# Optimization experiments

Measured on AMD Instinct MI355X. Metric: run time of the kernel, lower is better.

## Reference

```python
import jax, jax.numpy as jnp
import numpy as np

B, LQ, E = 4, 8400, 256
HEADS, LEVELS, POINTS = 8, 4, 4
HEAD_DIM = E // HEADS
SHAPES = [(80, 80), (40, 40), (20, 20), (10, 10)]  # (H, W) per level; sum HW = 8400
LV = sum(h * w for h, w in SHAPES)


def setup_inputs() -> dict:
    key = jax.random.key(0)
    ks = jax.random.split(key, 12)
    query = jax.random.normal(ks[0], (B, LQ, E), jnp.float32)
    # per-level normalized reference points in (0.1, 0.9)
    reference_points = 0.1 + 0.8 * jax.random.uniform(ks[1], (B, LQ, LEVELS, 2), jnp.float32)
    value = jax.random.normal(ks[2], (B, LV, E), jnp.float32)
    spatial_shapes = jnp.array(SHAPES, dtype=jnp.int32)
    s = 0.05
    Wv = jax.random.normal(ks[3], (E, E), jnp.float32) * s
    bv = jnp.zeros((E,), jnp.float32)
    Woff = jax.random.normal(ks[4], (E, HEADS * LEVELS * POINTS * 2), jnp.float32) * 0.01
    boff = jax.random.normal(ks[5], (HEADS * LEVELS * POINTS * 2,), jnp.float32) * 0.02
    Wattn = jax.random.normal(ks[6], (E, HEADS * LEVELS * POINTS), jnp.float32) * s
    battn = jnp.zeros((HEADS * LEVELS * POINTS,), jnp.float32)
    Wo = jax.random.normal(ks[7], (E, E), jnp.float32) * s
    bo = jnp.zeros((E,), jnp.float32)
    return dict(query=query, reference_points=reference_points, value=value,
                spatial_shapes=spatial_shapes, Wv=Wv, bv=bv, Woff=Woff, boff=boff,
                Wattn=Wattn, battn=battn, Wo=Wo, bo=bo)


def _bilinear_sample(vflat, x, y, Hl, Wl):
    # vflat: [BH, D, Hl*Wl]; x, y: [BH, N] pixel coords (align_corners=False convention)
    x0f = jnp.floor(x); y0f = jnp.floor(y)
    wx = (x - x0f)[:, None, :]; wy = (y - y0f)[:, None, :]
    x0 = x0f.astype(jnp.int32); y0 = y0f.astype(jnp.int32)

    def gather(ix, iy):
        valid = ((ix >= 0) & (ix < Wl) & (iy >= 0) & (iy < Hl)).astype(vflat.dtype)
        idx = jnp.clip(iy, 0, Hl - 1) * Wl + jnp.clip(ix, 0, Wl - 1)
        g = jnp.take_along_axis(vflat, idx[:, None, :], axis=2)  # [BH, D, N]
        return g * valid[:, None, :]

    v00 = gather(x0, y0); v01 = gather(x0 + 1, y0)
    v10 = gather(x0, y0 + 1); v11 = gather(x0 + 1, y0 + 1)
    return (v00 * (1 - wx) * (1 - wy) + v01 * wx * (1 - wy)
            + v10 * (1 - wx) * wy + v11 * wx * wy)


def _msda_forward(query, reference_points, value, spatial_shapes,
                  Wv, bv, Woff, boff, Wattn, battn, Wo, bo):
    b, lq, _ = query.shape
    v = (value @ Wv + bv).reshape(b, -1, HEADS, HEAD_DIM)
    off = (query @ Woff + boff).reshape(b, lq, HEADS, LEVELS, POINTS, 2)
    aw = (query @ Wattn + battn).reshape(b, lq, HEADS, LEVELS * POINTS)
    aw = jax.nn.softmax(aw, axis=-1).reshape(b, lq, HEADS, LEVELS, POINTS)
    # normalizer (W, H) per level
    norm = jnp.stack([spatial_shapes[:, 1], spatial_shapes[:, 0]], axis=-1).astype(query.dtype)
    # sampling locations in [0,1]: [B, Lq, H, L, P, 2]
    loc = reference_points[:, :, None, :, None, :] + off / norm[None, None, None, :, None, :]

    sampled_levels = []
    start = 0
    for lvl, (Hl, Wl) in enumerate(SHAPES):
        vl = v[:, start:start + Hl * Wl]                      # [B, Hl*Wl, H, D]
        start += Hl * Wl
        vflat = vl.transpose(0, 2, 3, 1).reshape(b * HEADS, HEAD_DIM, Hl * Wl)
        grid = loc[:, :, :, lvl]                              # [B, Lq, H, P, 2]
        grid = grid.transpose(0, 2, 1, 3, 4).reshape(b * HEADS, lq * POINTS, 2)
        g = grid * 2.0 - 1.0                                  # grid_sample convention
        x = (g[..., 0] + 1.0) * (Wl * 0.5) - 0.5
        y = (g[..., 1] + 1.0) * (Hl * 0.5) - 0.5
        s = _bilinear_sample(vflat, x, y, Hl, Wl)             # [BH, D, Lq*P]
        sampled_levels.append(s.reshape(b, HEADS, HEAD_DIM, lq, POINTS))
    sampled = jnp.stack(sampled_levels, axis=-1)              # [B, H, D, Lq, P, L]
    out = jnp.einsum('bhdqpl,bqhlp->bqhd', sampled, aw).reshape(b, lq, E)
    return out @ Wo + bo


def reference(query, reference_points, value, spatial_shapes,
              Wv, bv, Woff, boff, Wattn, battn, Wo, bo):
    return _msda_forward(query, reference_points, value, spatial_shapes,
                         Wv, bv, Woff, boff, Wattn, battn, Wo, bo)
```

## Files before the change

kernel.cpp:

```cpp
#include <hip/hip_runtime.h>
#include <math.h>

#define BB 4
#define LQ 8400
#define NH 8
#define LVTOT 8500
#define HD 32
#define PLANE_USH 544000

typedef __attribute__((ext_vector_type(8))) short short8;
typedef __attribute__((ext_vector_type(4))) float f32x4;
typedef __attribute__((ext_vector_type(2))) _Float16 half2_t;
typedef __attribute__((ext_vector_type(2))) __fp16 fp16x2_t;
typedef unsigned short ushort_t;

__device__ __forceinline__ ushort_t f2bf(float f) {
    union { float f; unsigned u; } v; v.f = f;
    unsigned r = v.u + 0x7fffu + ((v.u >> 16) & 1u);
    return (ushort_t)(r >> 16);
}
__device__ __forceinline__ float bflo(unsigned u) {
    union { unsigned u; float f; } x; x.u = u << 16; return x.f;
}
__device__ __forceinline__ float bfhi(unsigned u) {
    union { unsigned u; float f; } x; x.u = u & 0xffff0000u; return x.f;
}
__device__ __forceinline__ half2_t ash2(unsigned u) {
    union { unsigned u; half2_t h; } x; x.u = u; return x.h;
}
__device__ __forceinline__ unsigned pk2u(fp16x2_t h) {
    union { fp16x2_t h; unsigned u; } x; x.h = h; return x.u;
}

__device__ __forceinline__ void dma16(const ushort_t* g, ushort_t* l) {
    __builtin_amdgcn_global_load_lds(
        (const __attribute__((address_space(1))) void*)g,
        (__attribute__((address_space(3))) void*)l, 16, 0, 0);
}

__device__ __forceinline__ void lvl_decomp(int pix, int& lb, int& y, int& x,
                                           int& rowp) {
    if (pix < 6400)      { y = pix / 80;            x = pix - y * 80;  rowp = 40; lb = 0; }
    else if (pix < 8000) { int r = pix - 6400; y = r / 40; x = r - y * 40; rowp = 20; lb = 3200; }
    else if (pix < 8400) { int r = pix - 8000; y = r / 20; x = r - y * 20; rowp = 10; lb = 4000; }
    else                 { int r = pix - 8400; y = r / 10; x = r - y * 10; rowp = 5;  lb = 4200; }
}

__global__ __launch_bounds__(256) void prep_all(
    const float* __restrict__ value, const float* __restrict__ query,
    const float* __restrict__ Wv, const float* __restrict__ Woff,
    const float* __restrict__ Wattn, const float* __restrict__ Wo,
    ushort_t* __restrict__ value_b, ushort_t* __restrict__ query_b,
    ushort_t* __restrict__ BT)
{
    const int bid = blockIdx.x;
    if (bid < 16900) {
        const float* src = (bid < 8500) ? value : query;
        ushort_t* dst = (bid < 8500) ? value_b : query_b;
        int i = (bid < 8500 ? bid : bid - 8500) * 256 + threadIdx.x;
        float4 f = ((const float4*)src)[i];
        ushort4 o;
        o.x = f2bf(f.x); o.y = f2bf(f.y); o.z = f2bf(f.z); o.w = f2bf(f.w);
        ((ushort4*)dst)[i] = o;
    } else {
        int idx = (bid - 16900) * 256 + threadIdx.x;
        int r = idx >> 8, k = idx & 255;
        float v;
        if (r < 256) v = Wv[k * 256 + r];
        else if (r < 640) {
            int n = r - 256;
            v = (n < 256) ? Woff[k * 256 + n] : Wattn[k * 128 + (n - 256)];
        } else v = Wo[k * 256 + (r - 640)];
        BT[idx] = f2bf(v);
    }
}

__device__ __forceinline__ void gemm_core64(
    const ushort_t* __restrict__ A, const ushort_t* __restrict__ B, int M,
    int m0, int n0, ushort_t* Asl, ushort_t* Bsl, f32x4 acc[2][4])
{
    const int tid  = threadIdx.x;
    const int wave = tid >> 6, lane = tid & 63;
    const int quad = lane >> 4, mr = lane & 15;
    const int wm   = (wave >> 1) * 32, wn = (wave & 1) * 64;
    const int oct  = lane >> 3;
    const int bseg = lane & 7;

    for (int k0 = 0; k0 < 256; k0 += 64) {
        __syncthreads();
        #pragma unroll
        for (int i = 0; i < 2; i++) {
            int m  = i * 32 + wave * 8 + oct;
            int gs = bseg ^ (m & 7);
            int am = min(m0 + m, M - 1);
            dma16(A + (size_t)am * 256 + k0 + gs * 8,
                  Asl + (i * 32 + wave * 8) * 64 + lane * 8);
        }
        #pragma unroll
        for (int i = 0; i < 4; i++) {
            int n  = i * 32 + wave * 8 + oct;
            int gs = bseg ^ (n & 7);
            dma16(B + (size_t)(n0 + n) * 256 + k0 + gs * 8,
                  Bsl + (i * 32 + wave * 8) * 64 + lane * 8);
        }
        __syncthreads();
        #pragma unroll
        for (int ks = 0; ks < 2; ks++) {
            short8 af[2], bf[4];
            const int ksl = ks * 4 + quad;
            #pragma unroll
            for (int i = 0; i < 2; i++) {
                int m = wm + i * 16 + mr;
                af[i] = *(const short8*)&Asl[m * 64 + (ksl ^ (m & 7)) * 8];
            }
            #pragma unroll
            for (int j = 0; j < 4; j++) {
                int n = wn + j * 16 + mr;
                bf[j] = *(const short8*)&Bsl[n * 64 + (ksl ^ (n & 7)) * 8];
            }
            #pragma unroll
            for (int i = 0; i < 2; i++)
                #pragma unroll
                for (int j = 0; j < 4; j++)
                    acc[i][j] = __builtin_amdgcn_mfma_f32_16x16x32_bf16(
                        af[i], bf[j], acc[i][j], 0, 0, 0);
        }
    }
}

__global__ __launch_bounds__(256, 4) void gemm_fused(
    const ushort_t* __restrict__ Av, const ushort_t* __restrict__ Aq,
    const ushort_t* __restrict__ BT,
    const float* __restrict__ bv, const float* __restrict__ boff,
    const float* __restrict__ battn,
    ushort_t* __restrict__ vperm, ushort_t* __restrict__ off_b,
    ushort_t* __restrict__ awl_b)
{
    __shared__ ushort_t smem[12288];
    ushort_t* Asl = smem;
    ushort_t* Bsl = smem + 4096;

    const int bid = blockIdx.x;
    int mode, m0, n0, M;
    const ushort_t *A, *B;
    if (bid < 1064) { mode = 0; m0 = (bid >> 1) * 64; n0 = (bid & 1) * 128;
                      A = Av; B = BT; M = 34000; }
    else { int b2 = bid - 1064;
           mode = 1; m0 = (b2 / 3) * 64; n0 = (b2 % 3) * 128;
           A = Aq; B = BT + 65536; M = 33600; }

    f32x4 acc[2][4];
    #pragma unroll
    for (int i = 0; i < 2; i++)
        #pragma unroll
        for (int j = 0; j < 4; j++) acc[i][j] = (f32x4){0.f, 0.f, 0.f, 0.f};

    gemm_core64(A, B, M, m0, n0, Asl, Bsl, acc);

    const int tid  = threadIdx.x;
    const int wave = tid >> 6, lane = tid & 63;
    const int quad = lane >> 4, mr = lane & 15;
    const int wm   = (wave >> 1) * 32, wn = (wave & 1) * 64;

    __syncthreads();
    #pragma unroll
    for (int i = 0; i < 2; i++) {
        #pragma unroll
        for (int j = 0; j < 4; j++) {
            const int lc = wn + j * 16 + mr;
            const int c  = n0 + lc;
            const float bias = (mode == 0) ? bv[c]
                              : (c < 256 ? boff[c] : battn[c - 256]);
            #pragma unroll
            for (int reg = 0; reg < 4; reg++) {
                const int rl = wm + i * 16 + quad * 4 + reg;
                float val = acc[i][j][reg] + bias;
                ushort_t u;
                if (mode == 0) { union { _Float16 h; ushort_t u; } cv;
                                 cv.h = (_Float16)val; u = cv.u; }
                else u = f2bf(val);
                smem[rl * 128 + (lc ^ ((rl & 3) << 3))] = u;
            }
        }
    }
    __syncthreads();

    if (mode == 1) {
        #pragma unroll
        for (int k = 0; k < 4; k++) {
            int sid = k * 256 + tid;
            int rl = sid >> 4, cc = (sid & 15) * 8;
            int row = m0 + rl;
            if (row >= M) continue;
            uint4 v = *(const uint4*)&smem[rl * 128 + (cc ^ ((rl & 3) << 3))];
            if (n0 < 256) *(uint4*)&off_b[(size_t)row * 256 + n0 + cc] = v;
            else          *(uint4*)&awl_b[(size_t)row * 128 + cc] = v;
        }
    } else {
        const int hb = n0 >> 5;
        #pragma unroll
        for (int k = 0; k < 8; k++) {
            int sid = k * 256 + tid;
            int unit = sid >> 5;
            if (unit >= 63) continue;
            int sub = sid & 31;
            int hh = sub >> 3, q = sub & 7;
            int copy = (unit >= 32) ? 1 : 0;
            int t = copy ? ((unit - 32) * 2 + 1) : (unit * 2);
            int row = m0 + t;
            if (row + 1 >= 34000) continue;
            int b = row / LVTOT, pix = row - b * LVTOT;
            int lb, y, x, rowp;
            lvl_decomp(pix, lb, y, x, rowp);
            if (copy && x >= 2 * rowp - 1) continue;
            int p = x >> 1;
            int pidx = copy * 4250 + lb + y * rowp + p;
            int h = hb + hh;
            uint2 a  = *(const uint2*)&smem[t * 128 +
                          ((hh * 32 + q * 4) ^ ((t & 3) << 3))];
            uint2 b2 = *(const uint2*)&smem[(t + 1) * 128 +
                          ((hh * 32 + q * 4) ^ (((t + 1) & 3) << 3))];
            uint4 o;
            o.x = (a.x & 0xffffu) | (b2.x << 16);
            o.y = (a.x >> 16)     | (b2.x & 0xffff0000u);
            o.z = (a.y & 0xffffu) | (b2.y << 16);
            o.w = (a.y >> 16)     | (b2.y & 0xffff0000u);
            *(uint4*)((char*)(vperm + (size_t)(b * NH + h) * PLANE_USH)
                      + (size_t)pidx * 128 + q * 16) = o;
        }
        {
            int pixsel = tid >> 7;
            int rem = tid & 127;
            int hh = rem >> 5, d = rem & 31;
            int t = pixsel ? 63 : 0;
            int row = m0 + t;
            if (row < 34000) {
                int b = row / LVTOT, pix = row - b * LVTOT;
                int lb, y, x, rowp;
                lvl_decomp(pix, lb, y, x, rowp);
                bool doit; int p, slot;
                if (!pixsel) { doit = (x >= 2);            p = (x - 2) >> 1; slot = 1; }
                else         { doit = (x < 2 * rowp - 1);  p = (x - 1) >> 1; slot = 0; }
                if (doit) {
                    int pidx = 4250 + lb + y * rowp + p;
                    int h = hb + hh;
                    vperm[(size_t)(b * NH + h) * PLANE_USH
                          + (size_t)pidx * 64 + d * 2 + slot] =
                        smem[t * 128 + ((hh * 32 + d) ^ ((t & 3) << 3))];
                }
            }
        }
    }
}

__global__ __launch_bounds__(256, 4) void gemm_out(
    const ushort_t* __restrict__ A, const ushort_t* __restrict__ BT,
    const float* __restrict__ bo, float* __restrict__ out)
{
    __shared__ ushort_t smem[12288];
    ushort_t* Asl = smem;
    ushort_t* Bsl = smem + 4096;

    const int m0 = (blockIdx.x >> 1) * 64;
    const int n0 = (blockIdx.x & 1) * 128;
    const int M = 33600;

    f32x4 acc[2][4];
    #pragma unroll
    for (int i = 0; i < 2; i++)
        #pragma unroll
        for (int j = 0; j < 4; j++) acc[i][j] = (f32x4){0.f, 0.f, 0.f, 0.f};

    gemm_core64(A, BT, M, m0, n0, Asl, Bsl, acc);

    const int tid  = threadIdx.x;
    const int wave = tid >> 6, lane = tid & 63;
    const int quad = lane >> 4, mr = lane & 15;
    const int half = wave >> 1;
    const int wn   = (wave & 1) * 64;
    float* fsm = (float*)smem;

    #pragma unroll
    for (int i = 0; i < 2; i++) {
        __syncthreads();
        #pragma unroll
        for (int j = 0; j < 4; j++) {
            const int lc = wn + j * 16 + mr;
            const float bias = bo[n0 + lc];
            #pragma unroll
            for (int reg = 0; reg < 4; reg++) {
                const int rloc = half * 16 + quad * 4 + reg;
                const int cs = lc ^ (quad << 4);
                fsm[rloc * 128 + cs] = acc[i][j][reg] + bias;
            }
        }
        __syncthreads();
        #pragma unroll
        for (int k = 0; k < 4; k++) {
            int sid = k * 256 + tid;
            int rloc = sid >> 5, cw = (sid & 31) * 4;
            int row = m0 + (rloc >> 4) * 32 + i * 16 + (rloc & 15);
            if (row >= M) continue;
            int q2 = (rloc >> 2) & 3;
            float4 v = *(const float4*)&fsm[rloc * 128 + (cw ^ (q2 << 4))];
            *(float4*)&out[(size_t)row * 256 + n0 + cw] = v;
        }
    }
}

__global__ __launch_bounds__(256) void msda_sample(
    const ushort_t* __restrict__ vperm, const ushort_t* __restrict__ off,
    const ushort_t* __restrict__ awl, const float* __restrict__ refp,
    ushort_t* __restrict__ sampled)
{
    __shared__ int4 s_wi[16 * 33];

    const int tid = threadIdx.x;
    const int bid = blockIdx.x;
    const int h   = bid & 7;
    const int r   = bid >> 3;
    const int b   = r / 263;
    const int c   = r - b * 263;
    const int q0b = c * 32;
    const size_t bq0 = (size_t)b * LQ + q0b;

    const int Hs[4]    = {80, 40, 20, 10};
    const int pbase[4] = {0, 3200, 4000, 4200};

    #pragma unroll
    for (int it = 0; it < 2; it++) {
        const int s  = it * 256 + tid;
        const int ql = s >> 4, lp = s & 15;
        const int l  = lp >> 2;
        const int qv = (q0b + ql < LQ) ? ql : 0;
        const size_t bq = bq0 + qv;
        const int Wl = Hs[l];

        unsigned od = *(const unsigned*)(off + bq * 256 + h * 32 + lp * 2);
        float ox = bflo(od), oy = bfhi(od);
        float lgt = bflo((unsigned)awl[bq * 128 + h * 16 + lp]);
        float e = __expf(lgt);
        float sum = e;
        sum += __shfl_xor(sum, 1, 16);
        sum += __shfl_xor(sum, 2, 16);
        sum += __shfl_xor(sum, 4, 16);
        sum += __shfl_xor(sum, 8, 16);
        float aw = e * __builtin_amdgcn_rcpf(sum);

        float2 rp = *(const float2*)(refp + bq * 8 + l * 2);
        float x = rp.x * (float)Wl + ox - 0.5f;
        float y = rp.y * (float)Wl + oy - 0.5f;
        float x0f = floorf(x), y0f = floorf(y);
        float wx = x - x0f, wy = y - y0f;
        int x0 = (int)x0f, y0 = (int)y0f;
        float hx0 = ((x0 >= 0) & (x0 < Wl)) ? (1.f - wx) : 0.f;
        float hx1 = ((x0 + 1 >= 0) & (x0 + 1 < Wl)) ? wx : 0.f;
        float vy0w = ((y0 >= 0) & (y0 < Wl)) ? (1.f - wy) * aw : 0.f;
        float vy1w = ((y0 + 1 >= 0) & (y0 + 1 < Wl)) ? wy * aw : 0.f;
        int px = min(max(x0, 0), Wl - 2);
        float pl, pr;
        if (x0 < px)      { pl = hx1; pr = 0.f; }
        else if (x0 > px) { pl = 0.f; pr = hx0; }
        else              { pl = hx0; pr = hx1; }
        int cy0 = min(max(y0, 0), Wl - 1);
        int cy1 = min(max(y0 + 1, 0), Wl - 1);
        const int copy = px & 1;
        const int p    = copy ? ((px - 1) >> 1) : (px >> 1);
        const int rowp = Wl >> 1;
        const int cb   = copy * 4250 + pbase[l] + p;
        const int otop = (cb + cy0 * rowp) << 7;
        const int obot = (cb + cy1 * rowp) << 7;
        unsigned wt = pk2u(__builtin_amdgcn_cvt_pkrtz(pl * vy0w, pr * vy0w));
        unsigned wb = pk2u(__builtin_amdgcn_cvt_pkrtz(pl * vy1w, pr * vy1w));
        s_wi[lp * 33 + ql] = make_int4((int)wt, (int)wb, otop, obot);
    }
    __syncthreads();

    const int ql  = tid >> 3;
    const int l8  = tid & 7;
    const int dby = l8 * 16;

    if (q0b + ql < LQ) {
        const char* plane = (const char*)(vperm + (size_t)(b * NH + h) * PLANE_USH);
        float a0 = 0.f, a1 = 0.f, a2 = 0.f, a3 = 0.f;
        #pragma unroll
        for (int pt = 0; pt < 16; pt++) {
            int4 wi = s_wi[pt * 33 + ql];
            uint4 vt = *(const uint4*)(plane + (unsigned)(wi.z + dby));
            uint4 vb = *(const uint4*)(plane + (unsigned)(wi.w + dby));
            half2_t wt = ash2((unsigned)wi.x);
            half2_t wb = ash2((unsigned)wi.y);
            a0 = __builtin_amdgcn_fdot2(wt, ash2(vt.x), a0, false);
            a0 = __builtin_amdgcn_fdot2(wb, ash2(vb.x), a0, false);
            a1 = __builtin_amdgcn_fdot2(wt, ash2(vt.y), a1, false);
            a1 = __builtin_amdgcn_fdot2(wb, ash2(vb.y), a1, false);
            a2 = __builtin_amdgcn_fdot2(wt, ash2(vt.z), a2, false);
            a2 = __builtin_amdgcn_fdot2(wb, ash2(vb.z), a2, false);
            a3 = __builtin_amdgcn_fdot2(wt, ash2(vt.w), a3, false);
            a3 = __builtin_amdgcn_fdot2(wb, ash2(vb.w), a3, false);
        }
        const size_t bq = bq0 + ql;
        ushort4 o;
        o.x = f2bf(a0); o.y = f2bf(a1);
        o.z = f2bf(a2); o.w = f2bf(a3);
        *(ushort4*)(sampled + bq * 256 + h * 32 + l8 * 4) = o;
    }
}

extern "C" void kernel_launch(void* const* d_in, const int* in_sizes, int n_in,
                              void* d_out, int out_size, void* d_ws, size_t ws_size,
                              hipStream_t stream) {
    const float* query = (const float*)d_in[0];
    const float* refp  = (const float*)d_in[1];
    const float* value = (const float*)d_in[2];
    const float* Wv    = (const float*)d_in[4];
    const float* bv    = (const float*)d_in[5];
    const float* Woff  = (const float*)d_in[6];
    const float* boff  = (const float*)d_in[7];
    const float* Wattn = (const float*)d_in[8];
    const float* battn = (const float*)d_in[9];
    const float* Wo    = (const float*)d_in[10];
    const float* bo    = (const float*)d_in[11];
    float* out = (float*)d_out;

    ushort_t* ws = (ushort_t*)d_ws;
    ushort_t* off_b   = ws;
    ushort_t* awl_b   = off_b + 8601600;
    ushort_t* value_b = awl_b + 4300800;
    ushort_t* query_b = value_b + 8704000;
    ushort_t* vperm_b = query_b + 8601600;
    ushort_t* BT      = vperm_b + 17408000;
    ushort_t* sampled_b = query_b;

    prep_all<<<dim3(17796), 256, 0, stream>>>(
        value, query, Wv, Woff, Wattn, Wo, value_b, query_b, BT);

    gemm_fused<<<dim3(1064 + 1575), 256, 0, stream>>>(
        value_b, query_b, BT, bv, boff, battn, vperm_b, off_b, awl_b);

    msda_sample<<<dim3(8 * 4 * 263), 256, 0, stream>>>(
        vperm_b, off_b, awl_b, refp, sampled_b);

    gemm_out<<<dim3(1050), 256, 0, stream>>>(
        sampled_b, BT + 163840, bo, out);
}
```

Baseline: 209.5 us.

## Fuse fp32-to-bf16 input conversion into the projection GEMM A-tile load

The separate pass that converted value and query to bf16 is removed. The GEMM now DMAs fp32 A tiles straight into LDS with an XOR swizzle and converts them to bf16 in registers just before the MFMA. This drops one full read and write of both activation tensors plus a prep pass over them, leaving only the small weight-transpose prep kernel. In exchange the GEMM moves twice as many A bytes from global memory, uses more LDS (which may lower occupancy), and does the conversion arithmetic inside the inner loop.

```diff
diff --git a/kernel.cpp b/kernel.cpp
--- a/kernel.cpp
+++ b/kernel.cpp
@@ -37,6 +37,11 @@
         (const __attribute__((address_space(1))) void*)g,
         (__attribute__((address_space(3))) void*)l, 16, 0, 0);
 }
+__device__ __forceinline__ void dma16g(const void* g, void* l) {
+    __builtin_amdgcn_global_load_lds(
+        (const __attribute__((address_space(1))) void*)g,
+        (__attribute__((address_space(3))) void*)l, 16, 0, 0);
+}
 
 __device__ __forceinline__ void lvl_decomp(int pix, int& lb, int& y, int& x,
                                            int& rowp) {
@@ -46,32 +51,83 @@
     else                 { int r = pix - 8400; y = r / 10; x = r - y * 10; rowp = 5;  lb = 4200; }
 }
 
-__global__ __launch_bounds__(256) void prep_all(
-    const float* __restrict__ value, const float* __restrict__ query,
+__global__ __launch_bounds__(256) void prep_bt(
     const float* __restrict__ Wv, const float* __restrict__ Woff,
     const float* __restrict__ Wattn, const float* __restrict__ Wo,
-    ushort_t* __restrict__ value_b, ushort_t* __restrict__ query_b,
     ushort_t* __restrict__ BT)
 {
-    const int bid = blockIdx.x;
-    if (bid < 16900) {
-        const float* src = (bid < 8500) ? value : query;
-        ushort_t* dst = (bid < 8500) ? value_b : query_b;
-        int i = (bid < 8500 ? bid : bid - 8500) * 256 + threadIdx.x;
-        float4 f = ((const float4*)src)[i];
-        ushort4 o;
-        o.x = f2bf(f.x); o.y = f2bf(f.y); o.z = f2bf(f.z); o.w = f2bf(f.w);
-        ((ushort4*)dst)[i] = o;
-    } else {
-        int idx = (bid - 16900) * 256 + threadIdx.x;
-        int r = idx >> 8, k = idx & 255;
-        float v;
-        if (r < 256) v = Wv[k * 256 + r];
-        else if (r < 640) {
-            int n = r - 256;
-            v = (n < 256) ? Woff[k * 256 + n] : Wattn[k * 128 + (n - 256)];
-        } else v = Wo[k * 256 + (r - 640)];
-        BT[idx] = f2bf(v);
+    int idx = blockIdx.x * 256 + threadIdx.x;
+    int r = idx >> 8, k = idx & 255;
+    float v;
+    if (r < 256) v = Wv[k * 256 + r];
+    else if (r < 640) {
+        int n = r - 256;
+        v = (n < 256) ? Woff[k * 256 + n] : Wattn[k * 128 + (n - 256)];
+    } else v = Wo[k * 256 + (r - 640)];
+    BT[idx] = f2bf(v);
+}
+
+__device__ __forceinline__ void gemm_core64_f32a(
+    const float* __restrict__ A, const ushort_t* __restrict__ B, int M,
+    int m0, int n0, float* Af, ushort_t* Bsl, f32x4 acc[2][4])
+{
+    const int tid  = threadIdx.x;
+    const int wave = tid >> 6, lane = tid & 63;
+    const int quad = lane >> 4, mr = lane & 15;
+    const int wm   = (wave >> 1) * 32, wn = (wave & 1) * 64;
+    const int oct  = lane >> 3;
+    const int bseg = lane & 7;
+    const int r4   = lane >> 4;
+    const int s16  = lane & 15;
+
+    for (int k0 = 0; k0 < 256; k0 += 64) {
+        __syncthreads();
+        #pragma unroll
+        for (int i = 0; i < 4; i++) {
+            int m  = i * 16 + wave * 4 + r4;
+            int gs = s16 ^ (m & 15);
+            int am = min(m0 + m, M - 1);
+            dma16g((const char*)A + (size_t)am * 1024 + (size_t)(k0 + gs * 4) * 4,
+                   (char*)Af + (i * 16 + wave * 4) * 256 + lane * 16);
+        }
+        #pragma unroll
+        for (int i = 0; i < 4; i++) {
+            int n  = i * 32 + wave * 8 + oct;
+            int gs = bseg ^ (n & 7);
+            dma16(B + (size_t)(n0 + n) * 256 + k0 + gs * 8,
+                  Bsl + (i * 32 + wave * 8) * 64 + lane * 8);
+        }
+        __syncthreads();
+        #pragma unroll
+        for (int ks = 0; ks < 2; ks++) {
+            short8 af[2], bf[4];
+            const int ksl = ks * 4 + quad;
+            #pragma unroll
+            for (int i = 0; i < 2; i++) {
+                int m  = wm + i * 16 + mr;
+                int p0 = (ksl * 2) ^ (m & 15);
+                int p1 = (ksl * 2 + 1) ^ (m & 15);
+                float4 lo = *(const float4*)&Af[m * 64 + p0 * 4];
+                float4 hi = *(const float4*)&Af[m * 64 + p1 * 4];
+                short8 a;
+                a[0] = (short)f2bf(lo.x); a[1] = (short)f2bf(lo.y);
+                a[2] = (short)f2bf(lo.z); a[3] = (short)f2bf(lo.w);
+                a[4] = (short)f2bf(hi.x); a[5] = (short)f2bf(hi.y);
+                a[6] = (short)f2bf(hi.z); a[7] = (short)f2bf(hi.w);
+                af[i] = a;
+            }
+            #pragma unroll
+            for (int j = 0; j < 4; j++) {
+                int n = wn + j * 16 + mr;
+                bf[j] = *(const short8*)&Bsl[n * 64 + (ksl ^ (n & 7)) * 8];
+            }
+            #pragma unroll
+            for (int i = 0; i < 2; i++)
+                #pragma unroll
+                for (int j = 0; j < 4; j++)
+                    acc[i][j] = __builtin_amdgcn_mfma_f32_16x16x32_bf16(
+                        af[i], bf[j], acc[i][j], 0, 0, 0);
+        }
     }
 }
 
@@ -129,20 +185,21 @@
 }
 
 __global__ __launch_bounds__(256, 4) void gemm_fused(
-    const ushort_t* __restrict__ Av, const ushort_t* __restrict__ Aq,
+    const float* __restrict__ Av, const float* __restrict__ Aq,
     const ushort_t* __restrict__ BT,
     const float* __restrict__ bv, const float* __restrict__ boff,
     const float* __restrict__ battn,
     ushort_t* __restrict__ vperm, ushort_t* __restrict__ off_b,
     ushort_t* __restrict__ awl_b)
 {
-    __shared__ ushort_t smem[12288];
-    ushort_t* Asl = smem;
-    ushort_t* Bsl = smem + 4096;
+    __shared__ ushort_t smem[16384];
+    float*    Af  = (float*)smem;
+    ushort_t* Bsl = smem + 8192;
 
     const int bid = blockIdx.x;
     int mode, m0, n0, M;
-    const ushort_t *A, *B;
+    const float* A;
+    const ushort_t* B;
     if (bid < 1064) { mode = 0; m0 = (bid >> 1) * 64; n0 = (bid & 1) * 128;
                       A = Av; B = BT; M = 34000; }
     else { int b2 = bid - 1064;
@@ -155,7 +212,7 @@
         #pragma unroll
         for (int j = 0; j < 4; j++) acc[i][j] = (f32x4){0.f, 0.f, 0.f, 0.f};
 
-    gemm_core64(A, B, M, m0, n0, Asl, Bsl, acc);
+    gemm_core64_f32a(A, B, M, m0, n0, Af, Bsl, acc);
 
     const int tid  = threadIdx.x;
     const int wave = tid >> 6, lane = tid & 63;
@@ -426,17 +483,14 @@
     ushort_t* ws = (ushort_t*)d_ws;
     ushort_t* off_b   = ws;
     ushort_t* awl_b   = off_b + 8601600;
-    ushort_t* value_b = awl_b + 4300800;
-    ushort_t* query_b = value_b + 8704000;
-    ushort_t* vperm_b = query_b + 8601600;
+    ushort_t* vperm_b = awl_b + 4300800;
     ushort_t* BT      = vperm_b + 17408000;
-    ushort_t* sampled_b = query_b;
-
-    prep_all<<<dim3(17796), 256, 0, stream>>>(
-        value, query, Wv, Woff, Wattn, Wo, value_b, query_b, BT);
+    ushort_t* sampled_b = BT + 229376;
+
+    prep_bt<<<dim3(896), 256, 0, stream>>>(Wv, Woff, Wattn, Wo, BT);
 
     gemm_fused<<<dim3(1064 + 1575), 256, 0, stream>>>(
-        value_b, query_b, BT, bv, boff, battn, vperm_b, off_b, awl_b);
+        value, query, BT, bv, boff, battn, vperm_b, off_b, awl_b);
 
     msda_sample<<<dim3(8 * 4 * 263), 256, 0, stream>>>(
         vperm_b, off_b, awl_b, refp, sampled_b);
```

Measured after the change: 207.1 us. About the same (-1.2%).
